# Optimization experiments

Hardware: AMD Instinct MI355X
Metric: run time of the kernel (lower is better)

## Reference

```python
import jax, jax.numpy as jnp
import numpy as np

PE_SIZE = 16

def sinusoidal_pe(d, t):
    # standard transformer sinusoidal positional encoding [t, d]
    pos = jnp.arange(t, dtype=jnp.float32)[:, None]
    div = jnp.exp(jnp.arange(0, d, 2, dtype=jnp.float32) * (-jnp.log(10000.0) / d))
    pe = jnp.zeros((t, d), dtype=jnp.float32)
    pe = pe.at[:, 0::2].set(jnp.sin(pos * div))
    pe = pe.at[:, 1::2].set(jnp.cos(pos * div))
    return pe

def setup_inputs() -> dict:
    key = jax.random.key(0)
    ks = jax.random.split(key, 12)
    B, T, N, F = 2, 256, 128, 16
    E, D, H = 1024, 128, 288
    inp = {
        'spikes': jax.random.normal(ks[0], (B, T, N, F), dtype=jnp.float32),
        'W_emb': jax.random.normal(ks[1], (F, D), dtype=jnp.float32) * (1.0 / np.sqrt(F)),
        'b_emb': jnp.zeros((D,), dtype=jnp.float32),
        'Ws1': jax.random.normal(ks[2], (D, D), dtype=jnp.float32) * (1.0 / np.sqrt(D)),
        'bs1': jnp.zeros((D,), dtype=jnp.float32),
        'Ws2': jax.random.normal(ks[3], (D, D), dtype=jnp.float32) * (1.0 / np.sqrt(D)),
        'bs2': jnp.zeros((D,), dtype=jnp.float32),
        'Wr1': jax.random.normal(ks[4], (D, D), dtype=jnp.float32) * (1.0 / np.sqrt(D)),
        'br1': jnp.zeros((D,), dtype=jnp.float32),
        'Wr2': jax.random.normal(ks[5], (D, D), dtype=jnp.float32) * (1.0 / np.sqrt(D)),
        'br2': jnp.zeros((D,), dtype=jnp.float32),
        'Wc1': jax.random.normal(ks[6], (H, H), dtype=jnp.float32) * (1.0 / np.sqrt(H)),
        'bc1': jnp.zeros((H,), dtype=jnp.float32),
        'Wc2': jax.random.normal(ks[7], (H, 5), dtype=jnp.float32) * (1.0 / np.sqrt(H)),
        'bc2': jnp.zeros((5,), dtype=jnp.float32),
        'send_edges': jax.random.randint(ks[8], (E,), 0, N, dtype=jnp.int64 if jax.config.read('jax_enable_x64') else jnp.int32),
        'recv_edges': jax.random.randint(ks[9], (E,), 0, N, dtype=jnp.int64 if jax.config.read('jax_enable_x64') else jnp.int32),
    }
    return inp

def reference(spikes, W_emb, b_emb, Ws1, bs1, Ws2, bs2, Wr1, br1, Wr2, br2,
              Wc1, bc1, Wc2, bc2, send_edges, recv_edges):
    b, t = spikes.shape[0], spikes.shape[1]
    # embedder: Linear feat->emb (shared for send/recv inputs)
    emb = spikes @ W_emb + b_emb                       # [b,t,N,D]
    # send/recv MLPs: ReLU after every Linear (2 layers)
    send = jax.nn.relu(jax.nn.relu(emb @ Ws1 + bs1) @ Ws2 + bs2)  # [b,t,N,D]
    recv = jax.nn.relu(jax.nn.relu(emb @ Wr1 + br1) @ Wr2 + br2)  # [b,t,N,D]
    # edge gather along node dim
    send_e = send[:, :, send_edges]                    # [b,t,E,D]
    recv_e = recv[:, :, recv_edges]                    # [b,t,E,D]
    # positional encoding, broadcast over batch and edges
    pe = sinusoidal_pe(PE_SIZE, t)                     # [t,PE]
    pe_b = jnp.broadcast_to(pe[None, :, None, :], (b, t, send_e.shape[2], PE_SIZE))
    send_cat = jnp.concatenate([send_e, pe_b], axis=-1)
    recv_cat = jnp.concatenate([recv_e, pe_b], axis=-1)
    # temporal offset pairing: sender at t+1, receiver at t
    full_emb = jnp.concatenate([send_cat[:, 1:], recv_cat[:, :-1]], axis=-1)  # [b,t-1,E,288]
    # combine MLP: Linear+ReLU, Linear (final bias zero-init, no activation)
    out = jax.nn.relu(full_emb @ Wc1 + bc1) @ Wc2 + bc2   # [b,t-1,E,5]
    return out
```

## Files before the change

### kernel.cpp

```cpp
#include <hip/hip_runtime.h>
#include <hip/hip_bf16.h>
#include <hip/hip_fp16.h>
#include <cstdint>
#include <cstddef>

typedef __attribute__((ext_vector_type(8))) short bf16x8;
typedef __attribute__((ext_vector_type(8))) _Float16 f16x8;
typedef __attribute__((ext_vector_type(4))) float f32x4;
typedef __attribute__((ext_vector_type(4))) unsigned u32x4;

__device__ inline unsigned short f2bf(float f) {
    __hip_bfloat16 h = __float2bfloat16(f);
    return __builtin_bit_cast(unsigned short, h);
}
__device__ inline unsigned short f2h(float f) {
    _Float16 h = (_Float16)f;
    return __builtin_bit_cast(unsigned short, h);
}
__device__ inline unsigned cvtpkrtz(float lo, float hi) {
    unsigned pk;
    asm("v_cvt_pkrtz_f16_f32 %0, %1, %2" : "=v"(pk) : "v"(lo), "v"(hi));
    return pk;
}

__global__ void prep_kernel(
    const float* __restrict__ W_emb, const float* __restrict__ b_emb,
    const float* __restrict__ Ws1, const float* __restrict__ bs1,
    const float* __restrict__ Wr1, const float* __restrict__ br1,
    const float* __restrict__ Ws2, const float* __restrict__ bs2,
    const float* __restrict__ Wr2, const float* __restrict__ br2,
    const float* __restrict__ Wc1, const float* __restrict__ bc1,
    const float* __restrict__ Wc2,
    const int* __restrict__ se, const int* __restrict__ re,
    float* __restrict__ P, float* __restrict__ bias1, float* __restrict__ bias2,
    unsigned short* __restrict__ wg1f, unsigned short* __restrict__ wg2f,
    unsigned short* __restrict__ wg3fT, unsigned short* __restrict__ wc2f,
    int* __restrict__ eidx, int* __restrict__ sidx, int* __restrict__ ridx)
{
    const int tid = threadIdx.x;

    if (blockIdx.x < 287) {
        __shared__ float sv[3][16], cv[3][16];
        const int base = blockIdx.x * 256;
        const int t0 = base / 288;
        if (tid < 48) {
            const int dt = tid >> 4, i = tid & 15;
            const int ii = i >> 1;
            const float div = expf(-1.1512925464970229f * (float)ii);
            const float ang = (float)(t0 + dt) * div;
            sv[dt][i] = sinf(ang);
            cv[dt][i] = cosf(ang);
        }
        __syncthreads();
        const int id = base + tid;
        if (id < 73440) {
            const int t = id / 288, ho = id % 288;
            const int dt = t - t0;
            float acc = bc1[ho];
#pragma unroll
            for (int i = 0; i < 8; i++) {
                acc += sv[dt + 1][2 * i] * Wc1[(size_t)(128 + 2 * i) * 288 + ho];
                acc += cv[dt + 1][2 * i] * Wc1[(size_t)(129 + 2 * i) * 288 + ho];
                acc += sv[dt][2 * i]     * Wc1[(size_t)(272 + 2 * i) * 288 + ho];
                acc += cv[dt][2 * i]     * Wc1[(size_t)(273 + 2 * i) * 288 + ho];
            }
            P[id] = acc;
        }
        return;
    }

    if (blockIdx.x == 755) {
        __shared__ int sse[1024], sre[1024];
        __shared__ int hist[1024];
        __shared__ int scn[256];
        for (int i = tid; i < 1024; i += 256) {
            sse[i] = se[i]; sre[i] = re[i]; hist[i] = 0;
        }
        __syncthreads();
        for (int i = tid; i < 1024; i += 256)
            atomicAdd(&hist[sse[i] * 8 + (sre[i] & 7)], 1);
        __syncthreads();
        int loc[4]; int s = 0;
#pragma unroll
        for (int j = 0; j < 4; j++) { loc[j] = s; s += hist[tid * 4 + j]; }
        scn[tid] = s;
        __syncthreads();
        for (int off = 1; off < 256; off <<= 1) {
            const int v = (tid >= off) ? scn[tid - off] : 0;
            __syncthreads();
            scn[tid] += v;
            __syncthreads();
        }
        const int excl = scn[tid] - s;
#pragma unroll
        for (int j = 0; j < 4; j++) hist[tid * 4 + j] = excl + loc[j];
        __syncthreads();
        for (int i = tid; i < 1024; i += 256) {
            const int key = sse[i] * 8 + (sre[i] & 7);
            const int slot = atomicAdd(&hist[key], 1);
            eidx[slot] = i; sidx[slot] = sse[i]; ridx[slot] = sre[i];
        }
        return;
    }

    int id = (blockIdx.x - 287) * 256 + tid;

    if (id < 8192) {
        const int y = id >> 12, r = id & 4095;
        const int f = r >> 9, l = (r >> 3) & 63, j = r & 7;
        const int k = ((l >> 4) << 3) + j;
        const int n = f * 16 + (l & 15);
        float v = 0.f;
        if (k < 16) {
            const float* Wx = y ? Wr1 : Ws1;
            for (int d = 0; d < 128; d++) v += W_emb[k * 128 + d] * Wx[d * 128 + n];
        }
        wg1f[id] = f2bf(v);
        return;
    }
    id -= 8192;

    if (id < 256) {
        const int y = id >> 7, c = id & 127;
        const float* Wx = y ? Wr1 : Ws1;
        float v = (y ? br1 : bs1)[c];
        for (int d = 0; d < 128; d++) v += b_emb[d] * Wx[d * 128 + c];
        bias1[id] = v;
        return;
    }
    id -= 256;

    if (id < 32768) {
        const int y = id >> 14, r = id & 16383;
        const int f = r >> 9, l = (r >> 3) & 63, j = r & 7;
        const int ks = f >> 3, nf = f & 7;
        const int k = ks * 32 + ((l >> 4) << 3) + j;
        const int n = nf * 16 + (l & 15);
        wg2f[id] = f2bf((y ? Wr2 : Ws2)[(size_t)k * 128 + n]);
        return;
    }
    id -= 32768;

    if (id < 256) {
        bias2[id] = (id < 128) ? bs2[id] : br2[id - 128];
        return;
    }
    id -= 256;

    if (id < 73728) {
        const int p = id / 36864, r = id % 36864;
        const int frag = r >> 9, l = (r >> 3) & 63, j = r & 7;
        const int mt = frag >> 2, ks = frag & 3;
        const int k = ks * 32 + ((l >> 4) << 3) + j;
        const int n = mt * 16 + (l & 15);
        wg3fT[id] = f2bf(Wc1[(size_t)(p * 144 + k) * 288 + n]);
        return;
    }
    id -= 73728;

    if (id < 4608) {
        const int j = id & 7, l = (id >> 3) & 63, ks = id >> 9;
        const int k = ks * 32 + ((l >> 4) << 3) + j;
        const int c = l & 15;
        wc2f[id] = (c < 5) ? f2h(Wc2[(size_t)k * 5 + c]) : (unsigned short)0;
    }
}

#define H1ROWB 272
#define H1YB   34816
#define H2BASE 69632
#define SROWB  592
#define SMATB  75776
#define LDS_B2 151552

__global__ __launch_bounds__(1024) void final5(
    const float* __restrict__ spikes,
    const unsigned short* __restrict__ wg1f, const float* __restrict__ bias1,
    const unsigned short* __restrict__ wg2f, const float* __restrict__ bias2,
    const unsigned short* __restrict__ wg3fT, const float* __restrict__ Pt,
    const unsigned short* __restrict__ wc2f, const float* __restrict__ bc2,
    const int* __restrict__ eidx, const int* __restrict__ sidx,
    const int* __restrict__ ridx, float* __restrict__ out)
{
    extern __shared__ unsigned char lds[];
    const int slice = blockIdx.x;
    const int b = slice / 255, t = slice % 255;
    const int tid = threadIdx.x, w = tid >> 6, l = tid & 63;
    const int lm = l & 15, lk = l >> 4;

    {
        const int y = w >> 3, rowblk = w & 7;
        const int tt = y ? t : t + 1;
        bf16x8 a0 = {0, 0, 0, 0, 0, 0, 0, 0};
        if (lk < 2) {
            const float* p = spikes +
                ((size_t)((b * 256 + tt) * 128 + rowblk * 16 + lm)) * 16 + lk * 8;
            const float4 v0 = *reinterpret_cast<const float4*>(p);
            const float4 v1 = *reinterpret_cast<const float4*>(p + 4);
            a0[0] = (short)f2bf(v0.x); a0[1] = (short)f2bf(v0.y);
            a0[2] = (short)f2bf(v0.z); a0[3] = (short)f2bf(v0.w);
            a0[4] = (short)f2bf(v1.x); a0[5] = (short)f2bf(v1.y);
            a0[6] = (short)f2bf(v1.z); a0[7] = (short)f2bf(v1.w);
        }
        f32x4 acc[8];
#pragma unroll
        for (int nf = 0; nf < 8; nf++) acc[nf] = (f32x4){0.f, 0.f, 0.f, 0.f};
#pragma unroll
        for (int nf = 0; nf < 8; nf++) {
            const bf16x8 bfr = *reinterpret_cast<const bf16x8*>(
                wg1f + y * 4096 + nf * 512 + l * 8);
            acc[nf] = __builtin_amdgcn_mfma_f32_16x16x32_bf16(a0, bfr, acc[nf], 0, 0, 0);
        }
        unsigned char* hb = lds + y * H1YB + (rowblk * 16 + lk * 4) * H1ROWB;
#pragma unroll
        for (int nf = 0; nf < 8; nf++) {
            const int c = nf * 16 + lm;
            const float add = bias1[y * 128 + c];
#pragma unroll
            for (int reg = 0; reg < 4; reg++)
                *reinterpret_cast<unsigned short*>(hb + reg * H1ROWB + c * 2) =
                    f2bf(fmaxf(acc[nf][reg] + add, 0.f));
        }
    }
    __syncthreads();

    {
        const int y = w >> 3, rowblk = w & 7;
        bf16x8 a[4];
#pragma unroll
        for (int ks = 0; ks < 4; ks++)
            a[ks] = *reinterpret_cast<const bf16x8*>(
                lds + y * H1YB + (rowblk * 16 + lm) * H1ROWB + ks * 64 + lk * 16);
        f32x4 acc[8];
#pragma unroll
        for (int nf = 0; nf < 8; nf++) acc[nf] = (f32x4){0.f, 0.f, 0.f, 0.f};
#pragma unroll
        for (int ks = 0; ks < 4; ks++)
#pragma unroll
            for (int nf = 0; nf < 8; nf++) {
                const bf16x8 bfr = *reinterpret_cast<const bf16x8*>(
                    wg2f + (size_t)y * 16384 + (size_t)(ks * 8 + nf) * 512 + l * 8);
                acc[nf] = __builtin_amdgcn_mfma_f32_16x16x32_bf16(a[ks], bfr, acc[nf], 0, 0, 0);
            }
        unsigned char* hb = lds + H2BASE + y * H1YB + (rowblk * 16 + lk * 4) * H1ROWB;
#pragma unroll
        for (int nf = 0; nf < 8; nf++) {
            const int c = nf * 16 + lm;
            const float add = bias2[y * 128 + c];
#pragma unroll
            for (int reg = 0; reg < 4; reg++)
                *reinterpret_cast<unsigned short*>(hb + reg * H1ROWB + c * 2) =
                    f2bf(fmaxf(acc[nf][reg] + add, 0.f));
        }
    }
    __syncthreads();

    const int rowg = w & 3, colg = w >> 2;
    const int p  = colg >> 1;
    const int mtb = (colg & 1) * 9;
    bf16x8 bfr[2][4];
#pragma unroll
    for (int half = 0; half < 2; half++)
#pragma unroll
        for (int ks = 0; ks < 4; ks++)
            bfr[half][ks] = *reinterpret_cast<const bf16x8*>(
                lds + H2BASE + p * H1YB +
                (rowg * 32 + half * 16 + lm) * H1ROWB + ks * 64 + lk * 16);
    f16x8 bfrag[9];
#pragma unroll
    for (int ks = 0; ks < 9; ks++)
        bfrag[ks] = *reinterpret_cast<const f16x8*>(wc2f + (ks * 64 + l) * 8);
    const float bias = (lm < 5) ? bc2[lm] : 0.f;
    int srw[4], rrw[4];
#pragma unroll
    for (int it = 0; it < 4; it++) {
        const int base = (w * 4 + it) * 16 + lm;
        srw[it] = sidx[base];
        rrw[it] = ridx[base];
    }
    __syncthreads();

    {
        unsigned char* mb0 = lds + p * SMATB + (rowg * 32 + lm) * SROWB;
        unsigned char* mb1 = mb0 + 16 * SROWB;
#pragma unroll
        for (int m9 = 0; m9 < 9; m9++) {
            const int mt = mtb + m9;
            f32x4 acc0 = {0.f, 0.f, 0.f, 0.f};
            f32x4 acc1 = {0.f, 0.f, 0.f, 0.f};
#pragma unroll
            for (int ks = 0; ks < 4; ks++) {
                const bf16x8 afr = *reinterpret_cast<const bf16x8*>(
                    wg3fT + ((size_t)(((p * 18 + mt) << 2) + ks) << 9) + l * 8);
                acc0 = __builtin_amdgcn_mfma_f32_16x16x32_bf16(afr, bfr[0][ks], acc0, 0, 0, 0);
                acc1 = __builtin_amdgcn_mfma_f32_16x16x32_bf16(afr, bfr[1][ks], acc1, 0, 0, 0);
            }
            const int c0 = mt * 16 + lk * 4;
            float4 pa = {0.f, 0.f, 0.f, 0.f};
            if (p) pa = *reinterpret_cast<const float4*>(Pt + (size_t)t * 288 + c0);
            const int boff = mt * 32 + lk * 8;
            uint2 wv;
            wv.x = cvtpkrtz(acc0[0] + pa.x, acc0[1] + pa.y);
            wv.y = cvtpkrtz(acc0[2] + pa.z, acc0[3] + pa.w);
            *reinterpret_cast<uint2*>(mb0 + boff) = wv;
            wv.x = cvtpkrtz(acc1[0] + pa.x, acc1[1] + pa.y);
            wv.y = cvtpkrtz(acc1[2] + pa.z, acc1[3] + pa.w);
            *reinterpret_cast<uint2*>(mb1 + boff) = wv;
        }
    }
    __syncthreads();

    {
        f32x4 acc[4];
#pragma unroll
        for (int it = 0; it < 4; it++) acc[it] = (f32x4){0.f, 0.f, 0.f, 0.f};

#pragma unroll
        for (int ks = 0; ks < 9; ks++) {
            u32x4 s4[4], r4[4];
#pragma unroll
            for (int it = 0; it < 4; it++) {
                s4[it] = *reinterpret_cast<const u32x4*>(
                    lds + srw[it] * SROWB + lk * 16 + ks * 64);
                r4[it] = *reinterpret_cast<const u32x4*>(
                    lds + SMATB + rrw[it] * SROWB + lk * 16 + ks * 64);
            }
#pragma unroll
            for (int it = 0; it < 4; it++) {
                u32x4 hw;
#pragma unroll
                for (int i = 0; i < 4; i++) {
                    unsigned hsum, hrel;
                    asm("v_pk_add_f16 %0, %1, %2" : "=v"(hsum) : "v"(s4[it][i]), "v"(r4[it][i]));
                    asm("v_pk_max_f16 %0, %1, 0"  : "=v"(hrel) : "v"(hsum));
                    hw[i] = hrel;
                }
                acc[it] = __builtin_amdgcn_mfma_f32_16x16x32_f16(
                    __builtin_bit_cast(f16x8, hw), bfrag[ks], acc[it], 0, 0, 0);
            }
        }
        if (lm < 5) {
#pragma unroll
            for (int it = 0; it < 4; it++) {
                const int base = (w * 4 + it) * 16 + lk * 4;
#pragma unroll
                for (int reg = 0; reg < 4; reg++) {
                    const int edge = eidx[base + reg];
                    out[((size_t)slice * 1024 + edge) * 5 + lm] = acc[it][reg] + bias;
                }
            }
        }
    }
}

extern "C" void kernel_launch(void* const* d_in, const int* in_sizes, int n_in,
                              void* d_out, int out_size, void* d_ws, size_t ws_size,
                              hipStream_t stream)
{
    const float* spikes = (const float*)d_in[0];
    const float* W_emb  = (const float*)d_in[1];
    const float* b_emb  = (const float*)d_in[2];
    const float* Ws1    = (const float*)d_in[3];
    const float* bs1    = (const float*)d_in[4];
    const float* Ws2    = (const float*)d_in[5];
    const float* bs2    = (const float*)d_in[6];
    const float* Wr1    = (const float*)d_in[7];
    const float* br1    = (const float*)d_in[8];
    const float* Wr2    = (const float*)d_in[9];
    const float* br2    = (const float*)d_in[10];
    const float* Wc1    = (const float*)d_in[11];
    const float* bc1    = (const float*)d_in[12];
    const float* Wc2    = (const float*)d_in[13];
    const float* bc2    = (const float*)d_in[14];
    const int*   se     = (const int*)d_in[15];
    const int*   re     = (const int*)d_in[16];

    float* out = (float*)d_out;
    float* ws  = (float*)d_ws;

    float*          P     = ws;
    float*          bias1 = ws + 73440;
    float*          bias2 = ws + 73696;
    unsigned short* wg1f  = (unsigned short*)(ws + 73952);
    unsigned short* wg2f  = (unsigned short*)(ws + 78048);
    unsigned short* wg3fT = (unsigned short*)(ws + 94432);
    unsigned short* wc2f  = (unsigned short*)(ws + 131296);
    int*            eidx  = (int*)(ws + 133600);
    int*            sidx  = (int*)(ws + 134624);
    int*            ridx  = (int*)(ws + 135648);

    const dim3 blk(256);

    (void)hipFuncSetAttribute(reinterpret_cast<const void*>(final5),
                              hipFuncAttributeMaxDynamicSharedMemorySize, LDS_B2);

    prep_kernel<<<756, blk, 0, stream>>>(
        W_emb, b_emb, Ws1, bs1, Wr1, br1, Ws2, bs2, Wr2, br2, Wc1, bc1, Wc2,
        se, re, P, bias1, bias2, wg1f, wg2f, wg3fT, wc2f, eidx, sidx, ridx);

    final5<<<510, dim3(1024), LDS_B2, stream>>>(
        spikes, wg1f, bias1, wg2f, bias2, wg3fT, P, wc2f, bc2,
        eidx, sidx, ridx, out);
}
```

Measured before the change: 49.57 us.

## Reorder edges for LDS banks, drop a barrier, double-buffer combine loads

The edge-sorting block now adds a per-16-edge insertion sort on a hash of the receiver index and interleaves the slots, so the gathered LDS rows in the combine stage are meant to spread across banks. A __syncthreads after the first MLP layer becomes only an LDS waitcnt, on the assumption that each wave reads only the hidden rows it wrote. The combine loop is manually software-pipelined with two register buffer sets, loading slice k+1 while computing slice k. The pipelining raises register pressure, and removing the barrier is safe only if no wave reads another wave's rows.

```diff
diff --git a/kernel.cpp b/kernel.cpp
--- a/kernel.cpp
+++ b/kernel.cpp
@@ -73,6 +73,7 @@
         __shared__ int sse[1024], sre[1024];
         __shared__ int hist[1024];
         __shared__ int scn[256];
+        __shared__ int le[1024], ls[1024], lr[1024];
         for (int i = tid; i < 1024; i += 256) {
             sse[i] = se[i]; sre[i] = re[i]; hist[i] = 0;
         }
@@ -98,7 +99,28 @@
         for (int i = tid; i < 1024; i += 256) {
             const int key = sse[i] * 8 + (sre[i] & 7);
             const int slot = atomicAdd(&hist[key], 1);
-            eidx[slot] = i; sidx[slot] = sse[i]; ridx[slot] = sre[i];
+            le[slot] = i; ls[slot] = sse[i]; lr[slot] = sre[i];
+        }
+        __syncthreads();
+        if (tid < 64) {
+            const int b0 = tid * 16;
+            int ord[16];
+#pragma unroll
+            for (int j = 0; j < 16; j++) ord[j] = j;
+            for (int a = 1; a < 16; a++) {
+                const int oa = ord[a];
+                const int ka = (5 * lr[b0 + oa]) & 7;
+                int bpos = a - 1;
+                while (bpos >= 0 && ((5 * lr[b0 + ord[bpos]]) & 7) > ka) {
+                    ord[bpos + 1] = ord[bpos]; bpos--;
+                }
+                ord[bpos + 1] = oa;
+            }
+            for (int j = 0; j < 16; j++) {
+                const int src = b0 + ord[j];
+                const int dst = b0 + (((j & 7) << 1) | (j >> 3));
+                eidx[dst] = le[src]; sidx[dst] = ls[src]; ridx[dst] = lr[src];
+            }
         }
         return;
     }
@@ -222,7 +244,7 @@
                     f2bf(fmaxf(acc[nf][reg] + add, 0.f));
         }
     }
-    __syncthreads();
+    asm volatile("s_waitcnt lgkmcnt(0)" ::: "memory");
 
     {
         const int y = w >> 3, rowblk = w & 7;
@@ -315,30 +337,49 @@
 #pragma unroll
         for (int it = 0; it < 4; it++) acc[it] = (f32x4){0.f, 0.f, 0.f, 0.f};
 
-#pragma unroll
-        for (int ks = 0; ks < 9; ks++) {
-            u32x4 s4[4], r4[4];
-#pragma unroll
-            for (int it = 0; it < 4; it++) {
-                s4[it] = *reinterpret_cast<const u32x4*>(
-                    lds + srw[it] * SROWB + lk * 16 + ks * 64);
-                r4[it] = *reinterpret_cast<const u32x4*>(
-                    lds + SMATB + rrw[it] * SROWB + lk * 16 + ks * 64);
-            }
-#pragma unroll
-            for (int it = 0; it < 4; it++) {
-                u32x4 hw;
-#pragma unroll
-                for (int i = 0; i < 4; i++) {
-                    unsigned hsum, hrel;
-                    asm("v_pk_add_f16 %0, %1, %2" : "=v"(hsum) : "v"(s4[it][i]), "v"(r4[it][i]));
-                    asm("v_pk_max_f16 %0, %1, 0"  : "=v"(hrel) : "v"(hsum));
-                    hw[i] = hrel;
-                }
-                acc[it] = __builtin_amdgcn_mfma_f32_16x16x32_f16(
-                    __builtin_bit_cast(f16x8, hw), bfrag[ks], acc[it], 0, 0, 0);
-            }
-        }
+        u32x4 sA[4], rA[4], sB[4], rB[4];
+
+#define LDD(S4, R4, KS)                                                       \
+        {                                                                     \
+            _Pragma("unroll")                                                 \
+            for (int it = 0; it < 4; it++) {                                  \
+                S4[it] = *reinterpret_cast<const u32x4*>(                     \
+                    lds + srw[it] * SROWB + lk * 16 + (KS) * 64);             \
+                R4[it] = *reinterpret_cast<const u32x4*>(                     \
+                    lds + SMATB + rrw[it] * SROWB + lk * 16 + (KS) * 64);     \
+            }                                                                 \
+        }
+#define CPD(S4, R4, KS)                                                       \
+        {                                                                     \
+            _Pragma("unroll")                                                 \
+            for (int it = 0; it < 4; it++) {                                  \
+                u32x4 hw;                                                     \
+                _Pragma("unroll")                                             \
+                for (int i = 0; i < 4; i++) {                                 \
+                    unsigned hsum, hrel;                                      \
+                    asm("v_pk_add_f16 %0, %1, %2"                             \
+                        : "=v"(hsum) : "v"(S4[it][i]), "v"(R4[it][i]));       \
+                    asm("v_pk_max_f16 %0, %1, 0" : "=v"(hrel) : "v"(hsum));   \
+                    hw[i] = hrel;                                             \
+                }                                                             \
+                acc[it] = __builtin_amdgcn_mfma_f32_16x16x32_f16(             \
+                    __builtin_bit_cast(f16x8, hw), bfrag[KS], acc[it], 0, 0, 0); \
+            }                                                                 \
+        }
+
+        LDD(sA, rA, 0);
+        LDD(sB, rB, 1); CPD(sA, rA, 0);
+        LDD(sA, rA, 2); CPD(sB, rB, 1);
+        LDD(sB, rB, 3); CPD(sA, rA, 2);
+        LDD(sA, rA, 4); CPD(sB, rB, 3);
+        LDD(sB, rB, 5); CPD(sA, rA, 4);
+        LDD(sA, rA, 6); CPD(sB, rB, 5);
+        LDD(sB, rB, 7); CPD(sA, rA, 6);
+        LDD(sA, rA, 8); CPD(sB, rB, 7);
+        CPD(sA, rA, 8);
+#undef LDD
+#undef CPD
+
         if (lm < 5) {
 #pragma unroll
             for (int it = 0; it < 4; it++) {
```

New measurement: 54.34 us. 9.6% more time.
